# Performance work log

Measured on AMD Instinct MI355X. Metric: run time of the kernel, lower is better.

Reference implementation:

```python
import jax, jax.numpy as jnp
import numpy as np

K_MASK = -2.3819763e+38
NUM_HEADS = 16
NUM_KV_HEADS = 8
FEATURES = 2048
HEAD_DIM = 128
WINDOW = 1024
SOFT_CAP = 50.0
B, T = 2, 2048


def apply_rope(inputs, positions, head_dim, max_wavelength=10000):
    # inputs: [B, T, N, H], positions: [B, T]
    fraction = 2 * jnp.arange(0, head_dim // 2) / head_dim
    timescale = max_wavelength ** fraction
    sinusoid_inp = positions[..., None] / timescale[None, None, :]  # [B,T,H/2]
    sinusoid_inp = sinusoid_inp[..., None, :]  # [B,T,1,H/2]
    sin = jnp.sin(sinusoid_inp)
    cos = jnp.cos(sinusoid_inp)
    first_half, second_half = jnp.split(inputs, 2, axis=-1)
    first_part = first_half * cos - second_half * sin
    second_part = second_half * cos + first_half * sin
    return jnp.concatenate([first_part, second_part], axis=-1).astype(inputs.dtype)


def setup_inputs() -> dict:
    key = jax.random.key(0)
    k1, k2, k3, k4 = jax.random.split(key, 4)
    std = 0.02
    x = jax.random.normal(k1, (B, T, FEATURES), dtype=jnp.float32)
    segment_pos = jnp.broadcast_to(jnp.arange(T, dtype=jnp.int32), (B, T))
    # causal prefill mask [B, T, T]
    attn_mask = jnp.broadcast_to(jnp.tril(jnp.ones((T, T), dtype=bool)), (B, T, T))
    wq = jax.random.normal(k2, (NUM_HEADS, FEATURES, HEAD_DIM), dtype=jnp.float32) * std
    wkv = jax.random.normal(k3, (2, NUM_KV_HEADS, FEATURES, HEAD_DIM), dtype=jnp.float32) * std
    wo = jax.random.normal(k4, (NUM_HEADS, HEAD_DIM, FEATURES), dtype=jnp.float32) * std
    return {"x": x, "segment_pos": segment_pos, "attn_mask": attn_mask,
            "wq": wq, "wkv": wkv, "wo": wo}


def reference(x, segment_pos, attn_mask, wq, wkv, wo):
    # Projections (GQA path: num_kv_heads != num_heads)
    q = jnp.einsum('BTD,NDH->BTNH', x, wq)              # [B,T,N,H]
    k = jnp.einsum('BSD,KDH->BSKH', x, wkv[0])          # [B,S,K,H]
    v = jnp.einsum('BSD,KDH->BSKH', x, wkv[1])          # [B,S,K,H]

    q = apply_rope(q, segment_pos, HEAD_DIM)
    q = q * HEAD_DIM ** (-0.5)
    k = apply_rope(k, segment_pos, HEAD_DIM)

    b, t, n, h = q.shape
    g = n // NUM_KV_HEADS
    qg = q.reshape(b, t, NUM_KV_HEADS, g, h)
    logits = jnp.einsum('BTKGH,BSKH->BTKGS', qg, k)
    s = logits.shape[-1]
    logits = logits.reshape(b, t, n, s)

    # soft cap
    logits = jnp.tanh(logits / SOFT_CAP) * SOFT_CAP

    # sliding-window mask combined with attn_mask
    cache_positions = jnp.arange(s)[None, None, :]
    sp = segment_pos[:, :, None]
    sliding_mask = (cache_positions >= sp - WINDOW + 1) & (cache_positions <= sp + WINDOW - 1)
    mask = sliding_mask & attn_mask  # [B,T,S]

    padded_logits = jnp.where(mask[:, :, None, :], logits, K_MASK)
    probs = jax.nn.softmax(padded_logits, axis=-1).astype(k.dtype)

    pg = probs.reshape(b, t, NUM_KV_HEADS, g, s)
    encoded = jnp.einsum('BTKGS,BSKH->BTKGH', pg, v).reshape(b, t, n, h)
    attn_output = jnp.einsum('BTNH,NHD->BTD', encoded, wo)
    return attn_output
```

## Files before the change

### kernel.cpp

```cpp
#include <hip/hip_runtime.h>

typedef unsigned short u16;
typedef unsigned int u32;
typedef __attribute__((ext_vector_type(8))) short bfx8;
typedef __attribute__((ext_vector_type(4))) float fx4;

static __device__ __forceinline__ float b2f(u16 u) {
    union { float f; u32 i; } c; c.i = ((u32)u) << 16; return c.f;
}
static __device__ __forceinline__ u16 f2b(float f) {
    union { float f; u32 i; } c; c.f = f;
    u32 r = c.i + 0x7FFFu + ((c.i >> 16) & 1u);
    return (u16)(r >> 16);
}
typedef const __attribute__((address_space(1))) unsigned int* gas1;
typedef __attribute__((address_space(3))) unsigned int* las3;
static __device__ __forceinline__ void gll16(const void* g, void* l) {
    __builtin_amdgcn_global_load_lds((gas1)g, (las3)l, 16, 0, 0);
}

__global__ __launch_bounds__(256) void k_convert_x(const float* __restrict__ x, u16* __restrict__ xb) {
    size_t i = ((size_t)blockIdx.x * 256 + threadIdx.x) * 8;
    float4 a = *(const float4*)(x + i);
    float4 b = *(const float4*)(x + i + 4);
    union { u16 e[8]; uint4 v; } o;
    o.e[0] = f2b(a.x); o.e[1] = f2b(a.y); o.e[2] = f2b(a.z); o.e[3] = f2b(a.w);
    o.e[4] = f2b(b.x); o.e[5] = f2b(b.y); o.e[6] = f2b(b.z); o.e[7] = f2b(b.w);
    *(uint4*)(xb + i) = o.v;
}

__global__ __launch_bounds__(256) void k_pack_w1(const float* __restrict__ wq, const float* __restrict__ wkv,
                                                 u16* __restrict__ wb1) {
    __shared__ float t[128 * 33];
    int ci = blockIdx.x;
    int k0 = blockIdx.y << 5;
    int c0 = ci << 7;
    const float* src;
    if (ci < 16)      src = wq  + (size_t)ci * 2048 * 128;
    else if (ci < 24) src = wkv + (size_t)(ci - 16) * 2048 * 128;
    else              src = wkv + (size_t)(8 + ci - 24) * 2048 * 128;
    int tid = threadIdx.x;
#pragma unroll
    for (int i = 0; i < 16; i++) {
        int idx = i * 256 + tid;
        int kk = idx >> 7, cc = idx & 127;
        t[cc * 33 + kk] = src[(size_t)(k0 + kk) * 128 + cc];
    }
    __syncthreads();
#pragma unroll
    for (int i = 0; i < 16; i++) {
        int idx = i * 256 + tid;
        int cc = idx >> 5, kk = idx & 31;
        wb1[(size_t)(c0 + cc) * 2048 + k0 + kk] = f2b(t[cc * 33 + kk]);
    }
}

__global__ __launch_bounds__(256) void k_pack_w2(const float* __restrict__ wo, u16* __restrict__ wb2) {
    __shared__ float t[128 * 33];
    int c0 = blockIdx.x << 7;
    int k0 = blockIdx.y << 5;
    int tid = threadIdx.x;
#pragma unroll
    for (int i = 0; i < 16; i++) {
        int idx = i * 256 + tid;
        int kk = idx >> 7, cc = idx & 127;
        t[cc * 33 + kk] = wo[(size_t)(k0 + kk) * 2048 + c0 + cc];
    }
    __syncthreads();
#pragma unroll
    for (int i = 0; i < 16; i++) {
        int idx = i * 256 + tid;
        int cc = idx >> 5, kk = idx & 31;
        wb2[(size_t)(c0 + cc) * 2048 + k0 + kk] = f2b(t[cc * 33 + kk]);
    }
}

template <int BM, int OUT_BF16>
__global__ __launch_bounds__(512, 2) void k_gemm256(const u16* __restrict__ A, const u16* __restrict__ Bt,
                                                    void* __restrict__ C, int M, int N, int K) {
    constexpr int MF = BM / 32;
    constexpr int NA = BM / 16;
    constexpr int FR = NA + 16;
    constexpr int LPW = FR / 8;
    __shared__ u16 lds[4 * FR * 512];

    int tid = threadIdx.x, wave = tid >> 6, lane = tid & 63;
    int quad = lane >> 4, l16 = lane & 15;
    int wm = wave >> 2, wn = wave & 3;

    int nwg = gridDim.x * gridDim.y;
    int bid = blockIdx.y * gridDim.x + blockIdx.x;
    int swz = (bid & 7) * (nwg >> 3) + (bid >> 3);
    int bx = swz % gridDim.x, by = swz / gridDim.x;
    int r0 = by * BM, c0 = bx << 8;

    fx4 zero = {0.f, 0.f, 0.f, 0.f};
    fx4 acc[MF][4];
#pragma unroll
    for (int m = 0; m < MF; m++)
#pragma unroll
        for (int n = 0; n < 4; n++) acc[m][n] = zero;

    const u16* gsrc[LPW];
#pragma unroll
    for (int j = 0; j < LPW; j++) {
        int fw = wave * LPW + j;
        gsrc[j] = (fw < NA ? A + (size_t)(r0 + fw * 16 + l16) * K
                           : Bt + (size_t)(c0 + (fw - NA) * 16 + l16) * K) + quad * 8;
    }
    u16* ldst = lds + wave * (LPW * 512);

    int NT = K >> 5;
#pragma unroll
    for (int p = 0; p < 3; p++)
#pragma unroll
        for (int j = 0; j < LPW; j++) gll16(gsrc[j] + p * 32, ldst + p * (FR * 512) + j * 512);

    for (int t = 0; t < NT; ++t) {
        int rem = NT - 1 - t;
        if (rem >= 2)      asm volatile("s_waitcnt vmcnt(%0)" : : "n"(2 * LPW) : "memory");
        else if (rem == 1) asm volatile("s_waitcnt vmcnt(%0)" : : "n"(LPW) : "memory");
        else               asm volatile("s_waitcnt vmcnt(0)" : : : "memory");
        __builtin_amdgcn_s_barrier();

        const u16* Fb = lds + (t & 3) * (FR * 512);
        const u16* Ab = Fb + wm * (MF * 512);
        const u16* Bb = Fb + (NA + wn * 4) * 512;
        bfx8 bf[4], af[4];
#pragma unroll
        for (int n = 0; n < 4; n++) bf[n] = *(const bfx8*)(Bb + n * 512 + lane * 8);
#pragma unroll
        for (int m = 0; m < 4; m++) af[m] = *(const bfx8*)(Ab + m * 512 + lane * 8);
        if (t + 3 < NT) {
            u16* dst = lds + ((t + 3) & 3) * (FR * 512) + wave * (LPW * 512);
#pragma unroll
            for (int j = 0; j < LPW; j++) gll16(gsrc[j] + (size_t)(t + 3) * 32, dst + j * 512);
        }
        __builtin_amdgcn_s_barrier();
        __builtin_amdgcn_s_setprio(1);
#pragma unroll
        for (int m = 0; m < 4; m++)
#pragma unroll
            for (int n = 0; n < 4; n++)
                acc[m][n] = __builtin_amdgcn_mfma_f32_16x16x32_bf16(af[m], bf[n], acc[m][n], 0, 0, 0);
        __builtin_amdgcn_s_setprio(0);
        if constexpr (MF == 8) {
            __builtin_amdgcn_s_barrier();
#pragma unroll
            for (int m = 0; m < 4; m++) af[m] = *(const bfx8*)(Ab + (4 + m) * 512 + lane * 8);
            __builtin_amdgcn_s_barrier();
            __builtin_amdgcn_s_setprio(1);
#pragma unroll
            for (int m = 0; m < 4; m++)
#pragma unroll
                for (int n = 0; n < 4; n++)
                    acc[4 + m][n] = __builtin_amdgcn_mfma_f32_16x16x32_bf16(af[m], bf[n], acc[4 + m][n], 0, 0, 0);
            __builtin_amdgcn_s_setprio(0);
        }
    }
#pragma unroll
    for (int m = 0; m < MF; m++)
#pragma unroll
        for (int n = 0; n < 4; n++) {
            int col = c0 + wn * 64 + n * 16 + l16;
#pragma unroll
            for (int r = 0; r < 4; r++) {
                int row = r0 + wm * (BM / 2) + m * 16 + quad * 4 + r;
                float v = acc[m][n][r];
                if (OUT_BF16) ((u16*)C)[(size_t)row * N + col] = f2b(v);
                else          ((float*)C)[(size_t)row * N + col] = v;
            }
        }
}

__global__ __launch_bounds__(256) void k_rope(const u16* __restrict__ qkv, u16* __restrict__ Qb,
                                              u16* __restrict__ Kb, u16* __restrict__ Vb) {
    __shared__ float sc[128];
    int bt = blockIdx.x;
    int b = bt >> 11, t = bt & 2047;
    const u16* row = qkv + (size_t)bt * 4096;
    int tid = threadIdx.x;
    float tf = (float)t;
    const float RS = 0.08838834764831845f;
    const float LT = 0.20762050593046f;
    if (tid < 64) {
        float ang = tf * exp2f(-LT * (float)tid);
        float s, c; sincosf(ang, &s, &c);
        sc[tid] = s; sc[tid + 64] = c;
    }
    __syncthreads();
#pragma unroll
    for (int i = 0; i < 4; i++) {
        int idx = tid + i * 256;
        int n = idx >> 6, hp = idx & 63;
        float x1 = b2f(row[n * 128 + hp]);
        float x2 = b2f(row[n * 128 + hp + 64]);
        float s = sc[hp], c = sc[hp + 64];
        size_t o = ((size_t)(b * 16 + n) * 2048 + t) * 128 + hp;
        Qb[o]      = f2b((x1 * c - x2 * s) * RS);
        Qb[o + 64] = f2b((x2 * c + x1 * s) * RS);
    }
#pragma unroll
    for (int i = 0; i < 2; i++) {
        int idx = tid + i * 256;
        int kh = idx >> 6, hp = idx & 63;
        float x1 = b2f(row[2048 + kh * 128 + hp]);
        float x2 = b2f(row[2048 + kh * 128 + hp + 64]);
        float s = sc[hp], c = sc[hp + 64];
        size_t o = ((size_t)(b * 8 + kh) * 2048 + t) * 128 + hp;
        Kb[o]      = f2b(x1 * c - x2 * s);
        Kb[o + 64] = f2b(x2 * c + x1 * s);
    }
#pragma unroll
    for (int i = 0; i < 4; i++) {
        int idx = tid + i * 256;
        int kh = idx >> 7, h = idx & 127;
        Vb[((size_t)(b * 8 + kh) * 2048 + t) * 128 + h] = row[3072 + idx];
    }
}

__global__ __launch_bounds__(256) void k_transpose_v(const u16* __restrict__ Vb, u16* __restrict__ Vt) {
    __shared__ u16 t[128 * 136];
    int bk = blockIdx.y;
    int t0 = blockIdx.x << 7;
    const u16* src = Vb + ((size_t)bk * 2048 + t0) * 128;
    u16* dst = Vt + (size_t)bk * 128 * 2048 + t0;
    int tid = threadIdx.x;
#pragma unroll
    for (int it = 0; it < 8; it++) {
        int ch = tid + it * 256;
        int tt = ch >> 4, c8 = (ch & 15) << 3;
        *(uint4*)(t + tt * 136 + c8) = *(const uint4*)(src + (size_t)tt * 128 + c8);
    }
    __syncthreads();
#pragma unroll
    for (int it = 0; it < 8; it++) {
        int ch = tid + it * 256;
        int h = ch >> 4, s8 = (ch & 15) << 3;
        union { uint4 v; u16 e[8]; } vv;
#pragma unroll
        for (int j = 0; j < 8; j++) vv.e[j] = t[(s8 + j) * 136 + h];
        *(uint4*)(dst + (size_t)h * 2048 + s8) = vv.v;
    }
}

__global__ __launch_bounds__(512, 4) void k_attn(const u16* __restrict__ Qb, const u16* __restrict__ Kb,
                                                 const u16* __restrict__ Vt, u16* __restrict__ enc) {
    __shared__ u16 Ks[2][16 * 512];
    __shared__ u16 Vs[2][16 * 512];
    __shared__ u16 Pl[8 * 1024];
    int t0 = blockIdx.x << 6;
    int kh = blockIdx.y, b = blockIdx.z;
    int tid = threadIdx.x, wave = tid >> 6, lane = tid & 63;
    int quad = lane >> 4, l16 = lane & 15;
    int n = (kh << 1) + (wave >> 2);
    int tw = t0 + ((wave & 3) << 4);
    const u16* Qp = Qb + (size_t)(b * 16 + n) * 2048 * 128;
    const u16* Kp = Kb + (size_t)(b * 8 + kh) * 2048 * 128;
    const u16* Vp = Vt + (size_t)(b * 8 + kh) * 128 * 2048;

    bfx8 aq[4];
#pragma unroll
    for (int kb = 0; kb < 4; kb++)
        aq[kb] = *(const bfx8*)(Qp + (size_t)(tw + l16) * 128 + kb * 32 + quad * 8);

    const u16* kgp[2]; const u16* vgp[2];
#pragma unroll
    for (int q = 0; q < 2; q++) {
        int f = wave * 2 + q;
        kgp[q] = Kp + (size_t)((f >> 2) * 16 + l16) * 128 + (f & 3) * 32 + quad * 8;
        vgp[q] = Vp + (size_t)((f >> 1) * 16 + l16) * 2048 + (f & 1) * 32 + quad * 8;
    }
    u16* Pw = Pl + wave * 1024;

    fx4 zero = {0.f, 0.f, 0.f, 0.f};
    fx4 o_acc[8];
#pragma unroll
    for (int hb = 0; hb < 8; hb++) o_acc[hb] = zero;
    float lsum[4] = {0.f, 0.f, 0.f, 0.f};

    const float C1 = 0.057707801635559f;
    const float C2 = 144.269504088896f;

    int s_lo = t0 - 1023; if (s_lo < 0) s_lo = 0;
    int ts0 = s_lo >> 6, ts1 = t0 >> 6;

#pragma unroll
    for (int q = 0; q < 2; q++) {
        int f = wave * 2 + q;
        gll16(kgp[q] + (size_t)(ts0 << 6) * 128, Ks[0] + f * 512);
        gll16(vgp[q] + (ts0 << 6), Vs[0] + f * 512);
    }

    for (int ts = ts0; ts <= ts1; ts++) {
        int cur = (ts - ts0) & 1;
        int s0 = ts << 6;
        __builtin_amdgcn_s_barrier();
        if (ts < ts1) {
            int s1 = (ts + 1) << 6;
#pragma unroll
            for (int q = 0; q < 2; q++) {
                int f = wave * 2 + q;
                gll16(kgp[q] + (size_t)s1 * 128, Ks[cur ^ 1] + f * 512);
                gll16(vgp[q] + s1, Vs[cur ^ 1] + f * 512);
            }
            asm volatile("s_waitcnt vmcnt(4)" : : : "memory");
        } else {
            asm volatile("s_waitcnt vmcnt(0)" : : : "memory");
        }
        __builtin_amdgcn_s_barrier();

        if (s0 <= tw + 15 && s0 + 63 >= tw - 1023) {
            const u16* Kc = Ks[cur];
            const u16* Vc = Vs[cur];
            bool full = (s0 + 63 <= tw) && (s0 >= tw - 1008);
            if (full) {
#pragma unroll
                for (int nb = 0; nb < 4; nb++) {
                    fx4 sacc = zero;
                    __builtin_amdgcn_s_setprio(1);
#pragma unroll
                    for (int kb = 0; kb < 4; kb++) {
                        bfx8 bk = *(const bfx8*)(Kc + (nb * 4 + kb) * 512 + lane * 8);
                        sacc = __builtin_amdgcn_mfma_f32_16x16x32_bf16(aq[kb], bk, sacc, 0, 0, 0);
                    }
                    __builtin_amdgcn_s_setprio(0);
                    int base0 = ((nb >> 1) * 64 + ((nb & 1) * 2 + (l16 >> 3)) * 16 + quad * 4) * 8 + (l16 & 7);
#pragma unroll
                    for (int r = 0; r < 4; r++) {
                        float u = __builtin_amdgcn_exp2f(sacc[r] * C1);
                        float p = __builtin_amdgcn_exp2f(-C2 * __builtin_amdgcn_rcpf(u + 1.f));
                        lsum[r] += p;
                        Pw[base0 + r * 8] = f2b(p);
                    }
                }
            } else {
#pragma unroll
                for (int nb = 0; nb < 4; nb++) {
                    int sb = s0 + (nb << 4);
                    int base0 = ((nb >> 1) * 64 + ((nb & 1) * 2 + (l16 >> 3)) * 16 + quad * 4) * 8 + (l16 & 7);
                    if (sb <= tw + 15 && sb + 15 >= tw - 1023) {
                        fx4 sacc = zero;
#pragma unroll
                        for (int kb = 0; kb < 4; kb++) {
                            bfx8 bk = *(const bfx8*)(Kc + (nb * 4 + kb) * 512 + lane * 8);
                            sacc = __builtin_amdgcn_mfma_f32_16x16x32_bf16(aq[kb], bk, sacc, 0, 0, 0);
                        }
                        int sg = sb + l16;
#pragma unroll
                        for (int r = 0; r < 4; r++) {
                            int tg = tw + quad * 4 + r;
                            float u = __builtin_amdgcn_exp2f(sacc[r] * C1);
                            float p = __builtin_amdgcn_exp2f(-C2 * __builtin_amdgcn_rcpf(u + 1.f));
                            p = (sg <= tg && sg >= tg - 1023) ? p : 0.f;
                            lsum[r] += p;
                            Pw[base0 + r * 8] = f2b(p);
                        }
                    } else {
#pragma unroll
                        for (int r = 0; r < 4; r++) Pw[base0 + r * 8] = 0;
                    }
                }
            }
            asm volatile("s_waitcnt lgkmcnt(0)" : : : "memory");
            __builtin_amdgcn_sched_barrier(0);
            bfx8 pf[2];
#pragma unroll
            for (int kk = 0; kk < 2; kk++)
                pf[kk] = *(const bfx8*)(Pw + kk * 512 + lane * 8);
            __builtin_amdgcn_s_setprio(1);
#pragma unroll
            for (int hb = 0; hb < 8; hb++)
#pragma unroll
                for (int kk = 0; kk < 2; kk++) {
                    bfx8 vf = *(const bfx8*)(Vc + (hb * 2 + kk) * 512 + lane * 8);
                    o_acc[hb] = __builtin_amdgcn_mfma_f32_16x16x32_bf16(pf[kk], vf, o_acc[hb], 0, 0, 0);
                }
            __builtin_amdgcn_s_setprio(0);
        }
    }
#pragma unroll
    for (int r = 0; r < 4; r++) {
#pragma unroll
        for (int off = 1; off < 16; off <<= 1)
            lsum[r] += __shfl_xor(lsum[r], off);
        lsum[r] = 1.0f / lsum[r];
    }
#pragma unroll
    for (int hb = 0; hb < 8; hb++) {
        int h = hb * 16 + l16;
#pragma unroll
        for (int r = 0; r < 4; r++) {
            int tg = tw + quad * 4 + r;
            enc[((size_t)(b * 2048 + tg) * 16 + n) * 128 + h] = f2b(o_acc[hb][r] * lsum[r]);
        }
    }
}

extern "C" void kernel_launch(void* const* d_in, const int* in_sizes, int n_in,
                              void* d_out, int out_size, void* d_ws, size_t ws_size,
                              hipStream_t stream) {
    const float* x   = (const float*)d_in[0];
    const float* wq  = (const float*)d_in[3];
    const float* wkv = (const float*)d_in[4];
    const float* wo  = (const float*)d_in[5];
    char* ws = (char*)d_ws;
    const size_t MiB = 1024 * 1024;
    u16* xb  = (u16*)(ws);
    u16* wb1 = (u16*)(ws + 16 * MiB);
    u16* qkv = (u16*)(ws + 32 * MiB);
    u16* Qb  = (u16*)(ws);
    u16* Kb  = (u16*)(ws + 16 * MiB);
    u16* Vb  = (u16*)(ws + 24 * MiB);
    u16* enc = (u16*)(ws + 32 * MiB);
    u16* wb2 = (u16*)(ws + 48 * MiB);
    u16* Vt  = (u16*)(ws + 56 * MiB);

    k_convert_x<<<4096, 256, 0, stream>>>(x, xb);
    k_pack_w1<<<dim3(32, 64), 256, 0, stream>>>(wq, wkv, wb1);
    k_gemm256<256, 1><<<dim3(16, 16), 512, 0, stream>>>(xb, wb1, qkv, 4096, 4096, 2048);
    k_rope<<<4096, 256, 0, stream>>>(qkv, Qb, Kb, Vb);
    k_transpose_v<<<dim3(16, 16), 256, 0, stream>>>(Vb, Vt);
    k_pack_w2<<<dim3(16, 64), 256, 0, stream>>>(wo, wb2);
    k_attn<<<dim3(32, 8, 2), 512, 0, stream>>>(Qb, Kb, Vt, enc);
    k_gemm256<128, 0><<<dim3(8, 32), 512, 0, stream>>>(enc, wb2, d_out, 4096, 2048, 2048);
}
```

Measured before the change: 357.5 us.

## Software-pipeline LDS fragment loads in GEMM main loop with register double buffering

The GEMM main loop now preloads the A/B fragments for the first k-step before the loop. Each iteration then reads the next step's fragments from LDS into registers while issuing MFMAs on the current ones, and uses one barrier per iteration instead of two to four. This is meant to hide LDS read latency behind MFMA work and cut barrier stalls. The cost is extra VGPR pressure from the doubled fragment registers, which could lower occupancy. The barrier protecting the 4-slot ring buffer also changes, so the reuse-distance safety depends on the 3-ahead prefetch.

```diff
diff --git a/kernel.cpp b/kernel.cpp
--- a/kernel.cpp
+++ b/kernel.cpp
@@ -116,46 +116,61 @@
 #pragma unroll
         for (int j = 0; j < LPW; j++) gll16(gsrc[j] + p * 32, ldst + p * (FR * 512) + j * 512);
 
+    asm volatile("s_waitcnt vmcnt(%0)" : : "n"(2 * LPW) : "memory");
+    __builtin_amdgcn_s_barrier();
+
+    bfx8 cbf[4], caf[4];
+#pragma unroll
+    for (int n = 0; n < 4; n++) cbf[n] = *(const bfx8*)(lds + (NA + wn * 4 + n) * 512 + lane * 8);
+#pragma unroll
+    for (int m = 0; m < 4; m++) caf[m] = *(const bfx8*)(lds + (wm * MF + m) * 512 + lane * 8);
+
     for (int t = 0; t < NT; ++t) {
-        int rem = NT - 1 - t;
-        if (rem >= 2)      asm volatile("s_waitcnt vmcnt(%0)" : : "n"(2 * LPW) : "memory");
-        else if (rem == 1) asm volatile("s_waitcnt vmcnt(%0)" : : "n"(LPW) : "memory");
-        else               asm volatile("s_waitcnt vmcnt(0)" : : : "memory");
-        __builtin_amdgcn_s_barrier();
-
         const u16* Fb = lds + (t & 3) * (FR * 512);
-        const u16* Ab = Fb + wm * (MF * 512);
-        const u16* Bb = Fb + (NA + wn * 4) * 512;
-        bfx8 bf[4], af[4];
-#pragma unroll
-        for (int n = 0; n < 4; n++) bf[n] = *(const bfx8*)(Bb + n * 512 + lane * 8);
-#pragma unroll
-        for (int m = 0; m < 4; m++) af[m] = *(const bfx8*)(Ab + m * 512 + lane * 8);
-        if (t + 3 < NT) {
-            u16* dst = lds + ((t + 3) & 3) * (FR * 512) + wave * (LPW * 512);
-#pragma unroll
-            for (int j = 0; j < LPW; j++) gll16(gsrc[j] + (size_t)(t + 3) * 32, dst + j * 512);
-        }
-        __builtin_amdgcn_s_barrier();
+        bfx8 nbf[4], naf[4], af1[4];
+        bool has_next = (t + 1 < NT);
+        if (has_next) {
+            if (t + 2 < NT) asm volatile("s_waitcnt vmcnt(%0)" : : "n"(LPW) : "memory");
+            else            asm volatile("s_waitcnt vmcnt(0)" : : : "memory");
+            __builtin_amdgcn_s_barrier();
+            if (t + 3 < NT) {
+                u16* dst = lds + ((t + 3) & 3) * (FR * 512) + wave * (LPW * 512);
+#pragma unroll
+                for (int j = 0; j < LPW; j++) gll16(gsrc[j] + (size_t)(t + 3) * 32, dst + j * 512);
+            }
+        }
+        if constexpr (MF == 8) {
+#pragma unroll
+            for (int m = 0; m < 4; m++) af1[m] = *(const bfx8*)(Fb + (wm * MF + 4 + m) * 512 + lane * 8);
+        }
+        if (has_next) {
+            const u16* Fn = lds + ((t + 1) & 3) * (FR * 512);
+#pragma unroll
+            for (int n = 0; n < 4; n++) nbf[n] = *(const bfx8*)(Fn + (NA + wn * 4 + n) * 512 + lane * 8);
+#pragma unroll
+            for (int m = 0; m < 4; m++) naf[m] = *(const bfx8*)(Fn + (wm * MF + m) * 512 + lane * 8);
+        }
         __builtin_amdgcn_s_setprio(1);
 #pragma unroll
         for (int m = 0; m < 4; m++)
 #pragma unroll
             for (int n = 0; n < 4; n++)
-                acc[m][n] = __builtin_amdgcn_mfma_f32_16x16x32_bf16(af[m], bf[n], acc[m][n], 0, 0, 0);
+                acc[m][n] = __builtin_amdgcn_mfma_f32_16x16x32_bf16(caf[m], cbf[n], acc[m][n], 0, 0, 0);
         __builtin_amdgcn_s_setprio(0);
         if constexpr (MF == 8) {
-            __builtin_amdgcn_s_barrier();
-#pragma unroll
-            for (int m = 0; m < 4; m++) af[m] = *(const bfx8*)(Ab + (4 + m) * 512 + lane * 8);
-            __builtin_amdgcn_s_barrier();
             __builtin_amdgcn_s_setprio(1);
 #pragma unroll
             for (int m = 0; m < 4; m++)
 #pragma unroll
                 for (int n = 0; n < 4; n++)
-                    acc[4 + m][n] = __builtin_amdgcn_mfma_f32_16x16x32_bf16(af[m], bf[n], acc[4 + m][n], 0, 0, 0);
+                    acc[4 + m][n] = __builtin_amdgcn_mfma_f32_16x16x32_bf16(af1[m], cbf[n], acc[4 + m][n], 0, 0, 0);
             __builtin_amdgcn_s_setprio(0);
+        }
+        if (has_next) {
+#pragma unroll
+            for (int n = 0; n < 4; n++) cbf[n] = nbf[n];
+#pragma unroll
+            for (int m = 0; m < 4; m++) caf[m] = naf[m];
         }
     }
 #pragma unroll
```

Result: no change. 352.1 us (-1.5%).

## Switch GEMMs to 32x32x16 MFMA with double-buffered register fragments

Applied to the files above, without the earlier changes.

Rewrites the bf16 GEMM kernel to use 32x32x16 MFMA instructions instead of 16x16x32, which changes the LDS fragment layout, the global-to-LDS source addressing and the accumulator/output mapping. The K loop is unrolled by two and ping-pongs between two register fragment sets, so LDS reads for the next step overlap the MFMAs of the current one. The goal is fewer LDS reads per MFMA and better hiding of LDS latency in both projection GEMMs. In exchange the larger accumulators and doubled fragment registers raise register pressure, and the 16-element strided output stores may be less coalesced.

```diff
diff --git a/kernel.cpp b/kernel.cpp
--- a/kernel.cpp
+++ b/kernel.cpp
@@ -4,6 +4,7 @@
 typedef unsigned int u32;
 typedef __attribute__((ext_vector_type(8))) short bfx8;
 typedef __attribute__((ext_vector_type(4))) float fx4;
+typedef __attribute__((ext_vector_type(16))) float fx16;
 
 static __device__ __forceinline__ float b2f(u16 u) {
     union { float f; u32 i; } c; c.i = ((u32)u) << 16; return c.f;
@@ -76,16 +77,16 @@
 }
 
 template <int BM, int OUT_BF16>
-__global__ __launch_bounds__(512, 2) void k_gemm256(const u16* __restrict__ A, const u16* __restrict__ Bt,
-                                                    void* __restrict__ C, int M, int N, int K) {
-    constexpr int MF = BM / 32;
-    constexpr int NA = BM / 16;
-    constexpr int FR = NA + 16;
+__global__ __launch_bounds__(512, 2) void k_gemm32(const u16* __restrict__ A, const u16* __restrict__ Bt,
+                                                   void* __restrict__ C, int M, int N, int K) {
+    constexpr int MG  = BM / 64;
+    constexpr int NAF = BM / 16;
+    constexpr int FR  = NAF + 16;
     constexpr int LPW = FR / 8;
     __shared__ u16 lds[4 * FR * 512];
 
     int tid = threadIdx.x, wave = tid >> 6, lane = tid & 63;
-    int quad = lane >> 4, l16 = lane & 15;
+    int l32 = lane & 31, lh = lane >> 5;
     int wm = wave >> 2, wn = wave & 3;
 
     int nwg = gridDim.x * gridDim.y;
@@ -94,19 +95,22 @@
     int bx = swz % gridDim.x, by = swz / gridDim.x;
     int r0 = by * BM, c0 = bx << 8;
 
-    fx4 zero = {0.f, 0.f, 0.f, 0.f};
-    fx4 acc[MF][4];
-#pragma unroll
-    for (int m = 0; m < MF; m++)
-#pragma unroll
-        for (int n = 0; n < 4; n++) acc[m][n] = zero;
+    fx16 acc[MG][2];
+#pragma unroll
+    for (int mg = 0; mg < MG; mg++)
+#pragma unroll
+        for (int ng = 0; ng < 2; ng++)
+#pragma unroll
+            for (int r = 0; r < 16; r++) acc[mg][ng][r] = 0.f;
 
     const u16* gsrc[LPW];
 #pragma unroll
     for (int j = 0; j < LPW; j++) {
         int fw = wave * LPW + j;
-        gsrc[j] = (fw < NA ? A + (size_t)(r0 + fw * 16 + l16) * K
-                           : Bt + (size_t)(c0 + (fw - NA) * 16 + l16) * K) + quad * 8;
+        const u16* base;
+        if (fw < NAF) base = A + (size_t)(r0 + (fw >> 1) * 32 + l32) * K + (fw & 1) * 16;
+        else { int g = fw - NAF; base = Bt + (size_t)(c0 + (g >> 1) * 32 + l32) * K + (g & 1) * 16; }
+        gsrc[j] = base + lh * 8;
     }
     u16* ldst = lds + wave * (LPW * 512);
 
@@ -116,57 +120,51 @@
 #pragma unroll
         for (int j = 0; j < LPW; j++) gll16(gsrc[j] + p * 32, ldst + p * (FR * 512) + j * 512);
 
-    for (int t = 0; t < NT; ++t) {
-        int rem = NT - 1 - t;
-        if (rem >= 2)      asm volatile("s_waitcnt vmcnt(%0)" : : "n"(2 * LPW) : "memory");
-        else if (rem == 1) asm volatile("s_waitcnt vmcnt(%0)" : : "n"(LPW) : "memory");
-        else               asm volatile("s_waitcnt vmcnt(0)" : : : "memory");
+    asm volatile("s_waitcnt vmcnt(%0)" : : "n"(2 * LPW) : "memory");
+    __builtin_amdgcn_s_barrier();
+
+    bfx8 aA[MG][2], bA[2][2], aB[MG][2], bB[2][2];
+#define RDFR(dA, dB, slot) { const u16* Fb = lds + (slot) * (FR * 512);                                    \
+    _Pragma("unroll") for (int mg = 0; mg < MG; mg++) _Pragma("unroll") for (int kk = 0; kk < 2; kk++)     \
+        dA[mg][kk] = *(const bfx8*)(Fb + ((wm * MG + mg) * 2 + kk) * 512 + lane * 8);                      \
+    _Pragma("unroll") for (int ng = 0; ng < 2; ng++) _Pragma("unroll") for (int kk = 0; kk < 2; kk++)      \
+        dB[ng][kk] = *(const bfx8*)(Fb + (NAF + (wn * 2 + ng) * 2 + kk) * 512 + lane * 8); }
+#define MFMAC(a, b) { __builtin_amdgcn_s_setprio(1);                                                       \
+    _Pragma("unroll") for (int kk = 0; kk < 2; kk++) _Pragma("unroll") for (int mg = 0; mg < MG; mg++)     \
+    _Pragma("unroll") for (int ng = 0; ng < 2; ng++)                                                       \
+        acc[mg][ng] = __builtin_amdgcn_mfma_f32_32x32x16_bf16(a[mg][kk], b[ng][kk], acc[mg][ng], 0, 0, 0); \
+    __builtin_amdgcn_s_setprio(0); }
+#define STAGE(tt) { u16* dst = lds + ((tt) & 3) * (FR * 512) + wave * (LPW * 512);                         \
+    _Pragma("unroll") for (int j = 0; j < LPW; j++) gll16(gsrc[j] + (size_t)(tt) * 32, dst + j * 512); }
+
+    RDFR(aA, bA, 0);
+    for (int t = 0; t < NT; t += 2) {
+        if (t + 2 < NT) asm volatile("s_waitcnt vmcnt(%0)" : : "n"(LPW) : "memory");
+        else            asm volatile("s_waitcnt vmcnt(0)" : : : "memory");
         __builtin_amdgcn_s_barrier();
-
-        const u16* Fb = lds + (t & 3) * (FR * 512);
-        const u16* Ab = Fb + wm * (MF * 512);
-        const u16* Bb = Fb + (NA + wn * 4) * 512;
-        bfx8 bf[4], af[4];
-#pragma unroll
-        for (int n = 0; n < 4; n++) bf[n] = *(const bfx8*)(Bb + n * 512 + lane * 8);
-#pragma unroll
-        for (int m = 0; m < 4; m++) af[m] = *(const bfx8*)(Ab + m * 512 + lane * 8);
-        if (t + 3 < NT) {
-            u16* dst = lds + ((t + 3) & 3) * (FR * 512) + wave * (LPW * 512);
-#pragma unroll
-            for (int j = 0; j < LPW; j++) gll16(gsrc[j] + (size_t)(t + 3) * 32, dst + j * 512);
-        }
+        if (t + 3 < NT) STAGE(t + 3);
+        RDFR(aB, bB, (t + 1) & 3);
+        MFMAC(aA, bA);
+        if (t + 3 < NT) asm volatile("s_waitcnt vmcnt(%0)" : : "n"(LPW) : "memory");
+        else            asm volatile("s_waitcnt vmcnt(0)" : : : "memory");
         __builtin_amdgcn_s_barrier();
-        __builtin_amdgcn_s_setprio(1);
-#pragma unroll
-        for (int m = 0; m < 4; m++)
-#pragma unroll
-            for (int n = 0; n < 4; n++)
-                acc[m][n] = __builtin_amdgcn_mfma_f32_16x16x32_bf16(af[m], bf[n], acc[m][n], 0, 0, 0);
-        __builtin_amdgcn_s_setprio(0);
-        if constexpr (MF == 8) {
-            __builtin_amdgcn_s_barrier();
-#pragma unroll
-            for (int m = 0; m < 4; m++) af[m] = *(const bfx8*)(Ab + (4 + m) * 512 + lane * 8);
-            __builtin_amdgcn_s_barrier();
-            __builtin_amdgcn_s_setprio(1);
-#pragma unroll
-            for (int m = 0; m < 4; m++)
-#pragma unroll
-                for (int n = 0; n < 4; n++)
-                    acc[4 + m][n] = __builtin_amdgcn_mfma_f32_16x16x32_bf16(af[m], bf[n], acc[4 + m][n], 0, 0, 0);
-            __builtin_amdgcn_s_setprio(0);
-        }
-    }
-#pragma unroll
-    for (int m = 0; m < MF; m++)
-#pragma unroll
-        for (int n = 0; n < 4; n++) {
-            int col = c0 + wn * 64 + n * 16 + l16;
-#pragma unroll
-            for (int r = 0; r < 4; r++) {
-                int row = r0 + wm * (BM / 2) + m * 16 + quad * 4 + r;
-                float v = acc[m][n][r];
+        if (t + 4 < NT) STAGE(t + 4);
+        if (t + 2 < NT) RDFR(aA, bA, (t + 2) & 3);
+        MFMAC(aB, bB);
+    }
+#undef RDFR
+#undef MFMAC
+#undef STAGE
+#pragma unroll
+    for (int mg = 0; mg < MG; mg++)
+#pragma unroll
+        for (int ng = 0; ng < 2; ng++) {
+            int col = c0 + wn * 64 + ng * 32 + l32;
+            int row0 = r0 + wm * (BM / 2) + mg * 32 + 4 * lh;
+#pragma unroll
+            for (int r = 0; r < 16; r++) {
+                int row = row0 + (r & 3) + 8 * (r >> 2);
+                float v = acc[mg][ng][r];
                 if (OUT_BF16) ((u16*)C)[(size_t)row * N + col] = f2b(v);
                 else          ((float*)C)[(size_t)row * N + col] = v;
             }
@@ -418,10 +416,10 @@
 
     k_convert_x<<<4096, 256, 0, stream>>>(x, xb);
     k_pack_w1<<<dim3(32, 64), 256, 0, stream>>>(wq, wkv, wb1);
-    k_gemm256<256, 1><<<dim3(16, 16), 512, 0, stream>>>(xb, wb1, qkv, 4096, 4096, 2048);
+    k_gemm32<256, 1><<<dim3(16, 16), 512, 0, stream>>>(xb, wb1, qkv, 4096, 4096, 2048);
     k_rope<<<4096, 256, 0, stream>>>(qkv, Qb, Kb, Vb);
     k_transpose_v<<<dim3(16, 16), 256, 0, stream>>>(Vb, Vt);
     k_pack_w2<<<dim3(16, 64), 256, 0, stream>>>(wo, wb2);
     k_attn<<<dim3(32, 8, 2), 512, 0, stream>>>(Qb, Kb, Vt, enc);
-    k_gemm256<128, 0><<<dim3(8, 32), 512, 0, stream>>>(enc, wb2, d_out, 4096, 2048, 2048);
-}
+    k_gemm32<128, 0><<<dim3(8, 32), 512, 0, stream>>>(enc, wb2, d_out, 4096, 2048, 2048);
+}
```

After: 372.2 us. +4.1%, slower.
